# Optimization experiments

Hardware: AMD Instinct MI355X
Metric: run time of the kernel (lower is better)

The kernel has to match this reference:

```python
import jax, jax.numpy as jnp
import numpy as np

N_NODES = 100000
N_EDGES = 3200000
D_IN, D_HID, D_OUT = 256, 256, 64


def setup_inputs() -> dict:
    key = jax.random.key(0)
    k1, k2, k3, k4, k5 = jax.random.split(key, 5)
    return {
        "features": jax.random.normal(k1, (N_NODES, D_IN), dtype=jnp.float32),
        "W1": jax.random.normal(k2, (D_IN, D_HID), dtype=jnp.float32) / np.sqrt(D_IN),
        "b1": jnp.zeros((D_HID,), dtype=jnp.float32),
        "W2": jax.random.normal(k3, (D_HID, D_OUT), dtype=jnp.float32) / np.sqrt(D_HID),
        "b2": jnp.zeros((D_OUT,), dtype=jnp.float32),
        "src": jax.random.randint(k4, (N_EDGES,), 0, N_NODES, dtype=jnp.int32),
        "dst": jax.random.randint(k5, (N_EDGES,), 0, N_NODES, dtype=jnp.int32),
    }


def _degree_norms(src, dst, n_nodes):
    # DGL GraphConv norm='both': D_out^{-1/2} on source side, D_in^{-1/2} on dest side,
    # degrees clamped to min 1 (allow_zero_in_degree=True keeps zero-degree nodes).
    ones = jnp.ones(src.shape[0], dtype=jnp.float32)
    out_deg = jnp.clip(jax.ops.segment_sum(ones, src, num_segments=n_nodes), 1.0)
    in_deg = jnp.clip(jax.ops.segment_sum(ones, dst, num_segments=n_nodes), 1.0)
    return out_deg ** -0.5, in_deg ** -0.5


def _graph_conv(x, W, b, src, dst, out_norm, in_norm, n_nodes):
    # symmetric-normalized SpMM: D_in^{-1/2} A D_out^{-1/2} X, then dense linear
    x = x * out_norm[:, None]
    agg = jax.ops.segment_sum(x[src], dst, num_segments=n_nodes)  # gather + scatter-add
    agg = agg * in_norm[:, None]
    return agg @ W + b


def reference(features, W1, b1, W2, b2, src, dst):
    n = features.shape[0]
    out_norm, in_norm = _degree_norms(src, dst, n)
    h = jax.nn.relu(_graph_conv(features, W1, b1, src, dst, out_norm, in_norm, n))
    h = _graph_conv(h, W2, b2, src, dst, out_norm, in_norm, n)
    return h
```

## Files before the change

### kernel.cpp

```cpp
#include <hip/hip_runtime.h>

typedef unsigned short u16;
typedef unsigned char u8;
typedef unsigned int u32;
typedef __attribute__((ext_vector_type(8))) short short8;
typedef __attribute__((ext_vector_type(4))) float f32x4;
typedef __attribute__((ext_vector_type(2))) float f32x2;

#define CHSZ 8192
#define BSH 9
#define FD_CAP 18432
#define SCB 128

#define GLOAD_LDS16(g, l) \
    __builtin_amdgcn_global_load_lds((const __attribute__((address_space(1))) void*)(g), \
                                     (__attribute__((address_space(3))) void*)(l), 16, 0, 0)

__device__ __forceinline__ float bf2f(u16 h) {
    return __uint_as_float(((u32)h) << 16);
}
__device__ __forceinline__ u16 f2bf(float f) {
    u32 u = __float_as_uint(f);
    u += 0x7fffu + ((u >> 16) & 1u);
    return (u16)(u >> 16);
}
__device__ __forceinline__ float bflo(u32 v) { return __uint_as_float(v << 16); }
__device__ __forceinline__ float bfhi(u32 v) { return __uint_as_float(v & 0xffff0000u); }
__device__ __forceinline__ u8 f2fp8(float f) {
    return (u8)(__builtin_amdgcn_cvt_pk_fp8_f32(f, f, 0, false) & 0xff);
}

__global__ __launch_bounds__(256) void k_pcount(const int* __restrict__ src,
                                                const int* __restrict__ dst,
                                                u32* __restrict__ cntD, u32* __restrict__ cntS,
                                                int E, int NC, int nbkt) {
    __shared__ u32 hd[256], hs[256];
    int ch = blockIdx.x, t = threadIdx.x;
    hd[t] = 0; hs[t] = 0;
    __syncthreads();
    int e0 = ch * CHSZ;
    int e1 = e0 + CHSZ; if (e1 > E) e1 = E;
    for (int i = e0 + t * 4; i < e1; i += 1024) {
        if (i + 4 <= e1) {
            int4 s4 = *(const int4*)&src[i];
            int4 d4 = *(const int4*)&dst[i];
            atomicAdd(&hs[(u32)s4.x >> BSH], 1u); atomicAdd(&hd[(u32)d4.x >> BSH], 1u);
            atomicAdd(&hs[(u32)s4.y >> BSH], 1u); atomicAdd(&hd[(u32)d4.y >> BSH], 1u);
            atomicAdd(&hs[(u32)s4.z >> BSH], 1u); atomicAdd(&hd[(u32)d4.z >> BSH], 1u);
            atomicAdd(&hs[(u32)s4.w >> BSH], 1u); atomicAdd(&hd[(u32)d4.w >> BSH], 1u);
        } else {
            for (int k = i; k < e1; ++k) {
                atomicAdd(&hs[(u32)src[k] >> BSH], 1u);
                atomicAdd(&hd[(u32)dst[k] >> BSH], 1u);
            }
        }
    }
    __syncthreads();
    if (t < nbkt) {
        cntD[(size_t)t * NC + ch] = hd[t];
        cntS[(size_t)t * NC + ch] = hs[t];
    }
}

__global__ __launch_bounds__(256) void k_scan1(const u32* __restrict__ cntD,
                                               const u32* __restrict__ cntS,
                                               u32* __restrict__ bsum, int len) {
    __shared__ u32 sh[256];
    const u32* __restrict__ a = blockIdx.y ? cntS : cntD;
    int seg = (len + SCB - 1) / SCB;
    int i0 = blockIdx.x * seg;
    int i1 = i0 + seg; if (i1 > len) i1 = len;
    u32 s = 0;
    for (int i = i0 + threadIdx.x; i < i1; i += 256) s += a[i];
    sh[threadIdx.x] = s; __syncthreads();
    for (int off = 128; off > 0; off >>= 1) {
        if (threadIdx.x < off) sh[threadIdx.x] += sh[threadIdx.x + off];
        __syncthreads();
    }
    if (threadIdx.x == 0) bsum[blockIdx.y * SCB + blockIdx.x] = sh[0];
}

__global__ __launch_bounds__(256) void k_scan2(u32* __restrict__ bsum) {
    __shared__ u32 sh[256];
    int t = threadIdx.x;
    int lane = t & (SCB - 1);
    u32 v = bsum[t];
    sh[t] = v; __syncthreads();
    for (int off = 1; off < SCB; off <<= 1) {
        u32 x = (lane >= off) ? sh[t - off] : 0;
        __syncthreads();
        sh[t] += x;
        __syncthreads();
    }
    bsum[t] = sh[t] - v;
}

__global__ __launch_bounds__(256) void k_scan3(u32* __restrict__ cntD,
                                               u32* __restrict__ cntS,
                                               const u32* __restrict__ bsum, int len) {
    __shared__ u32 sh[256];
    u32* __restrict__ a = blockIdx.y ? cntS : cntD;
    int seg = (len + SCB - 1) / SCB;
    int i0 = blockIdx.x * seg;
    int i1 = i0 + seg; if (i1 > len) i1 = len;
    int per = (seg + 255) >> 8;
    int j0 = i0 + threadIdx.x * per;
    int j1 = j0 + per; if (j1 > i1) j1 = i1; if (j0 > i1) j0 = i1;
    u32 s = 0;
    for (int i = j0; i < j1; ++i) s += a[i];
    sh[threadIdx.x] = s; __syncthreads();
    for (int off = 1; off < 256; off <<= 1) {
        u32 x = (threadIdx.x >= off) ? sh[threadIdx.x - off] : 0;
        __syncthreads();
        sh[threadIdx.x] += x;
        __syncthreads();
    }
    u32 run = bsum[blockIdx.y * SCB + blockIdx.x] + (threadIdx.x ? sh[threadIdx.x - 1] : 0);
    for (int i = j0; i < j1; ++i) { u32 v = a[i]; a[i] = run; run += v; }
}

__global__ __launch_bounds__(256) void k_pscatter(const int* __restrict__ src,
                                                  const int* __restrict__ dst,
                                                  const u32* __restrict__ cntD,
                                                  const u32* __restrict__ cntS,
                                                  u32* __restrict__ partD, u16* __restrict__ partS,
                                                  int E, int NC, int nbkt) {
    __shared__ u32 bd[256], bs[256], rd[256], rs[256];
    int ch = blockIdx.x, t = threadIdx.x;
    if (t < nbkt) {
        bd[t] = cntD[(size_t)t * NC + ch];
        bs[t] = cntS[(size_t)t * NC + ch];
    }
    rd[t] = 0; rs[t] = 0;
    __syncthreads();
    int e0 = ch * CHSZ;
    int e1 = e0 + CHSZ; if (e1 > E) e1 = E;
    for (int i = e0 + t * 4; i < e1; i += 1024) {
        int lim = e1 - i; if (lim > 4) lim = 4;
        int sv[4], dv[4];
        if (lim == 4) {
            int4 s4 = *(const int4*)&src[i];
            int4 d4 = *(const int4*)&dst[i];
            sv[0] = s4.x; sv[1] = s4.y; sv[2] = s4.z; sv[3] = s4.w;
            dv[0] = d4.x; dv[1] = d4.y; dv[2] = d4.z; dv[3] = d4.w;
        } else {
            for (int j = 0; j < lim; ++j) { sv[j] = src[i + j]; dv[j] = dst[i + j]; }
        }
        for (int j = 0; j < lim; ++j) {
            u32 s = (u32)sv[j], d = (u32)dv[j];
            u32 kb = d >> BSH;
            u32 r = atomicAdd(&rd[kb], 1u);
            partD[bd[kb] + r] = (s << BSH) | (d & 511u);
            u32 sb = s >> BSH;
            u32 r2 = atomicAdd(&rs[sb], 1u);
            partS[bs[sb] + r2] = (u16)(s & 511u);
        }
    }
}

__global__ __launch_bounds__(256) void k_fin_dst(const u32* __restrict__ partD,
                                                 const u32* __restrict__ cntD,
                                                 int* __restrict__ rp, float* __restrict__ inorm,
                                                 int* __restrict__ es, int E, int NC, int nbkt, int N) {
    __shared__ u32 eb[FD_CAP];
    __shared__ u32 cnt[512], excl[512], cur[512], tmp[512];
    int b = blockIdx.x, t = threadIdx.x;
    int start = (int)cntD[(size_t)b * NC];
    int end = (b + 1 < nbkt) ? (int)cntD[(size_t)(b + 1) * NC] : E;
    int M = end - start;
    for (int i = t; i < 512; i += 256) { cnt[i] = 0; cur[i] = 0; }
    int Ml = M < FD_CAP ? M : FD_CAP;
    for (int i = t; i < Ml; i += 256) eb[i] = partD[start + i];
    __syncthreads();
    for (int i = t; i < M; i += 256) {
        u32 e = (i < FD_CAP) ? eb[i] : partD[start + i];
        atomicAdd(&cnt[e & 511u], 1u);
    }
    __syncthreads();
    tmp[t] = cnt[t]; tmp[t + 256] = cnt[t + 256];
    __syncthreads();
    for (int off = 1; off < 512; off <<= 1) {
        int i0 = t, i1 = t + 256;
        u32 v0 = tmp[i0] + ((i0 >= off) ? tmp[i0 - off] : 0);
        u32 v1 = tmp[i1] + ((i1 >= off) ? tmp[i1 - off] : 0);
        __syncthreads();
        tmp[i0] = v0; tmp[i1] = v1;
        __syncthreads();
    }
    excl[t] = tmp[t] - cnt[t]; excl[t + 256] = tmp[t + 256] - cnt[t + 256];
    __syncthreads();
    int lo = b << BSH;
    for (int i = t; i < 512; i += 256) {
        int node = lo + i;
        if (node < N) {
            rp[node] = start + (int)excl[i];
            u32 c = cnt[i]; if (c < 1u) c = 1u;
            inorm[node] = 1.0f / sqrtf((float)c);
        }
    }
    if (b == nbkt - 1 && t == 0) rp[N] = E;
    __syncthreads();
    for (int i = t; i < M; i += 256) {
        u32 e = (i < FD_CAP) ? eb[i] : partD[start + i];
        u32 d9 = e & 511u;
        u32 r = atomicAdd(&cur[d9], 1u);
        es[start + (int)excl[d9] + (int)r] = (int)((e >> BSH) << 7);
    }
}

__global__ __launch_bounds__(256) void k_fin_src(const u16* __restrict__ partS,
                                                 const u32* __restrict__ cntS,
                                                 float* __restrict__ onorm,
                                                 int E, int NC, int nbkt, int N) {
    __shared__ u32 c[512];
    int b = blockIdx.x, t = threadIdx.x;
    int start = (int)cntS[(size_t)b * NC];
    int end = (b + 1 < nbkt) ? (int)cntS[(size_t)(b + 1) * NC] : E;
    for (int i = t; i < 512; i += 256) c[i] = 0;
    __syncthreads();
    for (int i = start + t; i < end; i += 256) atomicAdd(&c[partS[i] & 511u], 1u);
    __syncthreads();
    int lo = b << BSH;
    for (int i = t; i < 512; i += 256) {
        int node = lo + i;
        if (node < N) {
            u32 v = c[i]; if (v < 1u) v = 1u;
            onorm[node] = 1.0f / sqrtf((float)v);
        }
    }
}

__global__ __launch_bounds__(256) void k_castx(const float* __restrict__ X,
                                               const float* __restrict__ onorm,
                                               u16* __restrict__ Xb, int total) {
    int stride = gridDim.x * blockDim.x * 4;
    for (int i = (blockIdx.x * blockDim.x + threadIdx.x) * 4; i < total; i += stride) {
        float4 v = *(const float4*)&X[i];
        float s = onorm[i >> 8];
        ushort4 o;
        o.x = f2bf(v.x * s); o.y = f2bf(v.y * s);
        o.z = f2bf(v.z * s); o.w = f2bf(v.w * s);
        *(ushort4*)&Xb[i] = o;
    }
}

__global__ void k_wt(const float* __restrict__ W, u16* __restrict__ Wt, int K, int C) {
    int i = blockIdx.x * 256 + threadIdx.x;
    if (i < K * C) {
        int k = i / C, c = i - k * C;
        Wt[(size_t)c * K + k] = f2bf(W[i]);
    }
}

template <int BN, int WM, int WN, int GWIN, int GWOUT, bool OFP8>
__global__ __launch_bounds__(256) void k_gemm(const u16* __restrict__ in,
                                              const u16* __restrict__ Wt,
                                              void* __restrict__ outv, int M) {
    constexpr int WTM = 128 / WM, WTN = BN / WN;
    constexpr int FM = WTM / 16, FN = WTN / 16;
    constexpr int BROUNDS = (BN * 64) / 4096;

    __shared__ u16 sA[128][32];
    __shared__ u16 sB[BN][32];

    int t = threadIdx.x, wid = t >> 6, l = t & 63;
    int wr = wid / WN, wc = wid % WN;
    int r0 = blockIdx.x * 128;
    int c0 = blockIdx.y * BN;

    f32x4 acc[FM][FN] = {};

    for (int kc = 0; kc < 256; kc += 32) {
#pragma unroll
        for (int r = 0; r < 2; ++r) {
            int off = r * 4096 + t * 16;
            int row = off >> 6;
            int ko = (off & 63) >> 1;
            int grow = r0 + row; if (grow >= M) grow = M - 1;
            const u16* gp;
            if constexpr (GWIN == 0)
                gp = in + (size_t)grow * 256 + kc + ko;
            else
                gp = in + ((size_t)(kc / GWIN) * M + grow) * GWIN + (kc % GWIN) + ko;
            GLOAD_LDS16(gp, (char*)&sA[0][0] + r * 4096 + wid * 1024);
        }
#pragma unroll
        for (int r = 0; r < BROUNDS; ++r) {
            int off = r * 4096 + t * 16;
            int col = off >> 6;
            int ko = (off & 63) >> 1;
            const u16* gp = Wt + (size_t)(c0 + col) * 256 + kc + ko;
            GLOAD_LDS16(gp, (char*)&sB[0][0] + r * 4096 + wid * 1024);
        }
        __syncthreads();

        short8 a[FM], b[FN];
#pragma unroll
        for (int m = 0; m < FM; ++m)
            a[m] = *(const short8*)&sA[wr * WTM + m * 16 + (l & 15)][(l >> 4) * 8];
#pragma unroll
        for (int n = 0; n < FN; ++n)
            b[n] = *(const short8*)&sB[wc * WTN + n * 16 + (l & 15)][(l >> 4) * 8];
#pragma unroll
        for (int m = 0; m < FM; ++m)
#pragma unroll
            for (int n = 0; n < FN; ++n)
                acc[m][n] = __builtin_amdgcn_mfma_f32_16x16x32_bf16(a[m], b[n], acc[m][n], 0, 0, 0);
        __syncthreads();
    }

#pragma unroll
    for (int m = 0; m < FM; ++m) {
#pragma unroll
        for (int n = 0; n < FN; ++n) {
#pragma unroll
            for (int e = 0; e < 4; ++e) {
                int row = r0 + wr * WTM + m * 16 + (l >> 4) * 4 + e;
                int col = c0 + wc * WTN + n * 16 + (l & 15);
                if (row < M) {
                    if constexpr (OFP8) {
                        u8* outp = (u8*)outv;
                        outp[((size_t)(col / GWOUT) * M + row) * GWOUT + (col % GWOUT)] =
                            f2fp8(acc[m][n][e]);
                    } else {
                        u16* outp = (u16*)outv;
                        u16 v = f2bf(acc[m][n][e]);
                        if constexpr (GWOUT == 0)
                            outp[(size_t)row * BN + col] = v;
                        else
                            outp[((size_t)(col / GWOUT) * M + row) * GWOUT + (col % GWOUT)] = v;
                    }
                }
            }
        }
    }
}

__global__ __launch_bounds__(256) void k_spmm1(const u8* __restrict__ A8,
                                               const int* __restrict__ rp,
                                               const int* __restrict__ es,
                                               const float* __restrict__ inorm,
                                               const float* __restrict__ onorm,
                                               const float* __restrict__ b1,
                                               u16* __restrict__ B2, int N) {
    int t = threadIdx.x, w = t >> 6, l = t & 63;
    int h = l >> 5, q = l & 31;
    int g = blockIdx.x & 1;
    int bi = blockIdx.x >> 1;
    int nb = gridDim.x >> 1;
    const u8* __restrict__ Ag = A8 + (size_t)g * N * 128;
    char* __restrict__ Bg = (char*)(B2 + (size_t)g * N * 128);
    float4 bias = *(const float4*)(b1 + g * 128 + q * 4);
    u32 qo4 = (u32)q * 4, qo8 = (u32)q * 8;

    for (int r0 = bi * 4; r0 < N; r0 += nb * 4) {
        int row = r0 + w;
        if (row >= N) continue;
        int beg = rp[row], end = rp[row + 1];
        float a0 = 0.f, a1 = 0.f, a2 = 0.f, a3 = 0.f;
        int i = beg;
        for (; i + 16 <= end; i += 16) {
            u32 s[8]; u32 v[8];
#pragma unroll
            for (int j = 0; j < 8; ++j) s[j] = (u32)es[i + 2 * j + h];
#pragma unroll
            for (int j = 0; j < 8; ++j) v[j] = *(const u32*)(Ag + s[j] + qo4);
#pragma unroll
            for (int j = 0; j < 8; ++j) {
                f32x2 lo = __builtin_amdgcn_cvt_pk_f32_fp8(v[j], false);
                f32x2 hi = __builtin_amdgcn_cvt_pk_f32_fp8(v[j], true);
                a0 += lo.x; a1 += lo.y; a2 += hi.x; a3 += hi.y;
            }
        }
        if (i < end) {
            int e0[8]; u32 s[8]; u32 v[8];
#pragma unroll
            for (int j = 0; j < 8; ++j) {
                e0[j] = i + 2 * j + h;
                s[j] = (u32)es[e0[j] < end ? e0[j] : beg];
            }
#pragma unroll
            for (int j = 0; j < 8; ++j) v[j] = *(const u32*)(Ag + s[j] + qo4);
#pragma unroll
            for (int j = 0; j < 8; ++j)
                if (e0[j] < end) {
                    f32x2 lo = __builtin_amdgcn_cvt_pk_f32_fp8(v[j], false);
                    f32x2 hi = __builtin_amdgcn_cvt_pk_f32_fp8(v[j], true);
                    a0 += lo.x; a1 += lo.y; a2 += hi.x; a3 += hi.y;
                }
        }
        a0 += __shfl_xor(a0, 32); a1 += __shfl_xor(a1, 32);
        a2 += __shfl_xor(a2, 32); a3 += __shfl_xor(a3, 32);
        if (h == 0) {
            float in_ = inorm[row], on_ = onorm[row];
            float h0 = fmaxf(in_ * a0 + bias.x, 0.f) * on_;
            float h1 = fmaxf(in_ * a1 + bias.y, 0.f) * on_;
            float h2 = fmaxf(in_ * a2 + bias.z, 0.f) * on_;
            float h3 = fmaxf(in_ * a3 + bias.w, 0.f) * on_;
            uint2 pk;
            pk.x = (u32)f2bf(h0) | ((u32)f2bf(h1) << 16);
            pk.y = (u32)f2bf(h2) | ((u32)f2bf(h3) << 16);
            *(uint2*)(Bg + (size_t)row * 256 + qo8) = pk;
        }
    }
}

__global__ __launch_bounds__(256) void k_spmm_out(const u16* __restrict__ Z,
                                                  const int* __restrict__ rp,
                                                  const int* __restrict__ es,
                                                  const float* __restrict__ inorm,
                                                  const float* __restrict__ bias,
                                                  float* __restrict__ out, int N) {
    int t = threadIdx.x, w = t >> 6, l = t & 63;
    int sub = l >> 4, q = l & 15;
    float4 bv = *(const float4*)(bias + q * 4);
    const char* __restrict__ Zc = (const char*)Z;
    u32 qo = (u32)q * 8;
    for (int r0 = blockIdx.x * 4; r0 < N; r0 += gridDim.x * 4) {
        int row = r0 + w;
        if (row >= N) continue;
        int beg = rp[row], end = rp[row + 1];
        float a0 = 0.f, a1 = 0.f, a2 = 0.f, a3 = 0.f;
        int i = beg;
        for (; i + 16 <= end; i += 16) {
            u32 s[4]; uint2 v[4];
#pragma unroll
            for (int j = 0; j < 4; ++j) s[j] = (u32)es[i + 4 * j + sub];
#pragma unroll
            for (int j = 0; j < 4; ++j) v[j] = *(const uint2*)(Zc + (s[j] + qo));
#pragma unroll
            for (int j = 0; j < 4; ++j) {
                a0 += bflo(v[j].x); a1 += bfhi(v[j].x);
                a2 += bflo(v[j].y); a3 += bfhi(v[j].y);
            }
        }
        if (i < end) {
            int e0[4]; u32 s[4]; uint2 v[4];
#pragma unroll
            for (int j = 0; j < 4; ++j) {
                e0[j] = i + 4 * j + sub;
                s[j] = (u32)es[e0[j] < end ? e0[j] : beg];
            }
#pragma unroll
            for (int j = 0; j < 4; ++j) v[j] = *(const uint2*)(Zc + (s[j] + qo));
#pragma unroll
            for (int j = 0; j < 4; ++j)
                if (e0[j] < end) {
                    a0 += bflo(v[j].x); a1 += bfhi(v[j].x);
                    a2 += bflo(v[j].y); a3 += bfhi(v[j].y);
                }
        }
        a0 += __shfl_xor(a0, 16); a1 += __shfl_xor(a1, 16);
        a2 += __shfl_xor(a2, 16); a3 += __shfl_xor(a3, 16);
        a0 += __shfl_xor(a0, 32); a1 += __shfl_xor(a1, 32);
        a2 += __shfl_xor(a2, 32); a3 += __shfl_xor(a3, 32);
        if (sub == 0) {
            float in_ = inorm[row];
            float4 o;
            o.x = in_ * a0 + bv.x; o.y = in_ * a1 + bv.y;
            o.z = in_ * a2 + bv.z; o.w = in_ * a3 + bv.w;
            *(float4*)(out + (size_t)row * 64 + q * 4) = o;
        }
    }
}

extern "C" void kernel_launch(void* const* d_in, const int* in_sizes, int n_in,
                              void* d_out, int out_size, void* d_ws, size_t ws_size,
                              hipStream_t stream) {
    const float* feat = (const float*)d_in[0];
    const float* W1   = (const float*)d_in[1];
    const float* b1   = (const float*)d_in[2];
    const float* W2   = (const float*)d_in[3];
    const float* b2   = (const float*)d_in[4];
    const int*   src  = (const int*)d_in[5];
    const int*   dst  = (const int*)d_in[6];

    const int DIN = 256;
    const int N = in_sizes[0] / DIN;
    const int E = in_sizes[5];
    float* out = (float*)d_out;

    const int NC = (E + CHSZ - 1) / CHSZ;
    const int NBKT = (N + 511) >> BSH;

    char* base = (char*)d_ws;
    size_t o = 0;
    auto take = [&](size_t b) { size_t r = o; o += (b + 255) & ~(size_t)255; return r; };
    u32* cntD = (u32*)(base + take((size_t)NBKT * NC * 4));
    u32* cntS = (u32*)(base + take((size_t)NBKT * NC * 4));
    u32* bsum = (u32*)(base + take((size_t)2 * SCB * 4));
    u32* partD = (u32*)(base + take((size_t)E * 4));
    u16* partS = (u16*)(base + take((size_t)E * 2));
    float* onorm = (float*)(base + take((size_t)N * 4));
    float* inorm = (float*)(base + take((size_t)N * 4));
    int* rp   = (int*)(base + take((size_t)(N + 1) * 4));
    u16* Wt1  = (u16*)(base + take((size_t)256 * 256 * 2));
    u16* Wt2  = (u16*)(base + take((size_t)64 * 256 * 2));
    int* es   = (int*)(base + take((size_t)E * 4));
    u16* S1   = (u16*)(base + take((size_t)N * 256 * 2));
    u16* S2   = (u16*)(base + take((size_t)N * 256 * 2));
    u16* S3   = (u16*)(base + take((size_t)N * 64 * 2));
    (void)ws_size; (void)n_in; (void)out_size;

    u16* Xb = S1;
    u8*  A8 = (u8*)S2;
    u16* B2 = S1;
    u16* Z  = S3;

    int len = NBKT * NC;
    k_pcount<<<NC, 256, 0, stream>>>(src, dst, cntD, cntS, E, NC, NBKT);
    dim3 gs(SCB, 2);
    k_scan1<<<gs, 256, 0, stream>>>(cntD, cntS, bsum, len);
    k_scan2<<<1, 256, 0, stream>>>(bsum);
    k_scan3<<<gs, 256, 0, stream>>>(cntD, cntS, bsum, len);
    k_pscatter<<<NC, 256, 0, stream>>>(src, dst, cntD, cntS, partD, partS, E, NC, NBKT);
    k_fin_src<<<NBKT, 256, 0, stream>>>(partS, cntS, onorm, E, NC, NBKT, N);
    k_fin_dst<<<NBKT, 256, 0, stream>>>(partD, cntD, rp, inorm, es, E, NC, NBKT, N);

    k_castx<<<8192, 256, 0, stream>>>(feat, onorm, Xb, N * 256);
    k_wt<<<(256 * 256 + 255) / 256, 256, 0, stream>>>(W1, Wt1, 256, 256);
    k_wt<<<(256 * 64 + 255) / 256, 256, 0, stream>>>(W2, Wt2, 256, 64);

    int mtiles = (N + 127) / 128;

    dim3 g1(mtiles, 2);
    k_gemm<128, 2, 2, 0, 128, true><<<g1, 256, 0, stream>>>(Xb, Wt1, A8, N);
    k_spmm1<<<8192, 256, 0, stream>>>(A8, rp, es, inorm, onorm, b1, B2, N);

    dim3 g2(mtiles, 1);
    k_gemm<64, 4, 1, 128, 0, false><<<g2, 256, 0, stream>>>(B2, Wt2, Z, N);
    k_spmm_out<<<8192, 256, 0, stream>>>(Z, rp, es, inorm, b2, out, N);
}
```

Measured before the change: 341.6 us.

## Split SpMM passes into per-column-group launches to shrink gather working set

```diff
diff --git a/kernel.cpp b/kernel.cpp
--- a/kernel.cpp
+++ b/kernel.cpp
@@ -342,12 +342,11 @@
                                                const float* __restrict__ inorm,
                                                const float* __restrict__ onorm,
                                                const float* __restrict__ b1,
-                                               u16* __restrict__ B2, int N) {
+                                               u16* __restrict__ B2, int N, int g) {
     int t = threadIdx.x, w = t >> 6, l = t & 63;
     int h = l >> 5, q = l & 31;
-    int g = blockIdx.x & 1;
-    int bi = blockIdx.x >> 1;
-    int nb = gridDim.x >> 1;
+    int bi = blockIdx.x;
+    int nb = gridDim.x;
     const u8* __restrict__ Ag = A8 + (size_t)g * N * 128;
     char* __restrict__ Bg = (char*)(B2 + (size_t)g * N * 128);
     float4 bias = *(const float4*)(b1 + g * 128 + q * 4);
@@ -405,61 +404,63 @@
     }
 }
 
-__global__ __launch_bounds__(256) void k_spmm_out(const u16* __restrict__ Z,
+__global__ __launch_bounds__(256) void k_spmm_out(const u16* __restrict__ Z2,
                                                   const int* __restrict__ rp,
                                                   const int* __restrict__ es,
                                                   const float* __restrict__ inorm,
                                                   const float* __restrict__ bias,
-                                                  float* __restrict__ out, int N) {
+                                                  float* __restrict__ out, int N, int g) {
     int t = threadIdx.x, w = t >> 6, l = t & 63;
-    int sub = l >> 4, q = l & 15;
-    float4 bv = *(const float4*)(bias + q * 4);
-    const char* __restrict__ Zc = (const char*)Z;
+    int j0 = l >> 3, q = l & 7;
+    const char* __restrict__ Zg = (const char*)(Z2 + (size_t)g * N * 32);
+    float4 bv = *(const float4*)(bias + g * 32 + q * 4);
     u32 qo = (u32)q * 8;
+
     for (int r0 = blockIdx.x * 4; r0 < N; r0 += gridDim.x * 4) {
         int row = r0 + w;
         if (row >= N) continue;
         int beg = rp[row], end = rp[row + 1];
         float a0 = 0.f, a1 = 0.f, a2 = 0.f, a3 = 0.f;
         int i = beg;
-        for (; i + 16 <= end; i += 16) {
+        for (; i + 32 <= end; i += 32) {
             u32 s[4]; uint2 v[4];
 #pragma unroll
-            for (int j = 0; j < 4; ++j) s[j] = (u32)es[i + 4 * j + sub];
-#pragma unroll
-            for (int j = 0; j < 4; ++j) v[j] = *(const uint2*)(Zc + (s[j] + qo));
+            for (int j = 0; j < 4; ++j) s[j] = (u32)es[i + 8 * j + j0] >> 1;
+#pragma unroll
+            for (int j = 0; j < 4; ++j) v[j] = *(const uint2*)(Zg + (s[j] + qo));
 #pragma unroll
             for (int j = 0; j < 4; ++j) {
                 a0 += bflo(v[j].x); a1 += bfhi(v[j].x);
                 a2 += bflo(v[j].y); a3 += bfhi(v[j].y);
             }
         }
+        for (; i + 8 <= end; i += 8) {
+            u32 s = (u32)es[i + j0] >> 1;
+            uint2 v = *(const uint2*)(Zg + (s + qo));
+            a0 += bflo(v.x); a1 += bfhi(v.x);
+            a2 += bflo(v.y); a3 += bfhi(v.y);
+        }
         if (i < end) {
-            int e0[4]; u32 s[4]; uint2 v[4];
-#pragma unroll
-            for (int j = 0; j < 4; ++j) {
-                e0[j] = i + 4 * j + sub;
-                s[j] = (u32)es[e0[j] < end ? e0[j] : beg];
+            int e0 = i + j0;
+            u32 s = (u32)es[e0 < end ? e0 : beg] >> 1;
+            uint2 v = *(const uint2*)(Zg + (s + qo));
+            if (e0 < end) {
+                a0 += bflo(v.x); a1 += bfhi(v.x);
+                a2 += bflo(v.y); a3 += bfhi(v.y);
             }
-#pragma unroll
-            for (int j = 0; j < 4; ++j) v[j] = *(const uint2*)(Zc + (s[j] + qo));
-#pragma unroll
-            for (int j = 0; j < 4; ++j)
-                if (e0[j] < end) {
-                    a0 += bflo(v[j].x); a1 += bfhi(v[j].x);
-                    a2 += bflo(v[j].y); a3 += bfhi(v[j].y);
-                }
-        }
+        }
+        a0 += __shfl_xor(a0, 8);  a1 += __shfl_xor(a1, 8);
+        a2 += __shfl_xor(a2, 8);  a3 += __shfl_xor(a3, 8);
         a0 += __shfl_xor(a0, 16); a1 += __shfl_xor(a1, 16);
         a2 += __shfl_xor(a2, 16); a3 += __shfl_xor(a3, 16);
         a0 += __shfl_xor(a0, 32); a1 += __shfl_xor(a1, 32);
         a2 += __shfl_xor(a2, 32); a3 += __shfl_xor(a3, 32);
-        if (sub == 0) {
+        if (j0 == 0) {
             float in_ = inorm[row];
             float4 o;
             o.x = in_ * a0 + bv.x; o.y = in_ * a1 + bv.y;
             o.z = in_ * a2 + bv.z; o.w = in_ * a3 + bv.w;
-            *(float4*)(out + (size_t)row * 64 + q * 4) = o;
+            *(float4*)(out + (size_t)row * 64 + g * 32 + q * 4) = o;
         }
     }
 }
@@ -505,7 +506,7 @@
     u16* Xb = S1;
     u8*  A8 = (u8*)S2;
     u16* B2 = S1;
-    u16* Z  = S3;
+    u16* Z2 = S3;
 
     int len = NBKT * NC;
     k_pcount<<<NC, 256, 0, stream>>>(src, dst, cntD, cntS, E, NC, NBKT);
@@ -523,11 +524,13 @@
 
     int mtiles = (N + 127) / 128;
 
-    dim3 g1(mtiles, 2);
-    k_gemm<128, 2, 2, 0, 128, true><<<g1, 256, 0, stream>>>(Xb, Wt1, A8, N);
-    k_spmm1<<<8192, 256, 0, stream>>>(A8, rp, es, inorm, onorm, b1, B2, N);
+    dim3 g1(mtiles, 1);
+    k_gemm<256, 2, 2, 0, 128, true><<<g1, 256, 0, stream>>>(Xb, Wt1, A8, N);
+    k_spmm1<<<8192, 256, 0, stream>>>(A8, rp, es, inorm, onorm, b1, B2, N, 0);
+    k_spmm1<<<8192, 256, 0, stream>>>(A8, rp, es, inorm, onorm, b1, B2, N, 1);
 
     dim3 g2(mtiles, 1);
-    k_gemm<64, 4, 1, 128, 0, false><<<g2, 256, 0, stream>>>(B2, Wt2, Z, N);
-    k_spmm_out<<<8192, 256, 0, stream>>>(Z, rp, es, inorm, b2, out, N);
-}
+    k_gemm<64, 4, 1, 128, 32, false><<<g2, 256, 0, stream>>>(B2, Wt2, Z2, N);
+    k_spmm_out<<<8192, 256, 0, stream>>>(Z2, rp, es, inorm, b2, out, N, 0);
+    k_spmm_out<<<8192, 256, 0, stream>>>(Z2, rp, es, inorm, b2, out, N, 1);
+}
```

New measurement: 416.1 us. +21.8%, slower.
